# Kernel tuning notes

Measured on AMD Instinct MI355X. Metric: run time of the kernel, lower is better.

## Reference

```python
import jax, jax.numpy as jnp
import numpy as np

NUM_ITERATIONS = 3


def squash(t, axis=-1):
    # scale * t / sqrt(||t||^2 + eps), scale = ||t||^2 / (1 + ||t||^2)
    sq = jnp.sum(t * t, axis=axis, keepdims=True)
    return (sq / (1.0 + sq)) * t / jnp.sqrt(sq + 1e-8)


def setup_inputs() -> dict:
    key = jax.random.key(0)
    k1, k2 = jax.random.split(key)
    B, C, R, I, O = 128, 10, 8192, 8, 16
    x = jax.random.normal(k1, (B, R, I), dtype=jnp.float32)
    route_weights = jax.random.normal(k2, (C, R, I, O), dtype=jnp.float32) * 0.1
    return {"x": x, "route_weights": route_weights}


def reference(x, route_weights):
    # x: [B, R, I]; route_weights: [C, R, I, O]
    u_hat = jnp.einsum('bri,crio->bcro', x, route_weights)  # [B, C, R, O]
    B, C, R, O = u_hat.shape
    b_ij = jnp.zeros((B, C, R), dtype=u_hat.dtype)
    v_j = None
    for it in range(NUM_ITERATIONS):
        c_ij = jax.nn.softmax(b_ij, axis=1)                 # [B, C, R]
        s_j = jnp.einsum('bcr,bcro->bco', c_ij, u_hat)      # [B, C, O]
        v_j = squash(s_j, axis=-1)                          # [B, C, O]
        if it < NUM_ITERATIONS - 1:
            a_ij = jnp.einsum('bcro,bco->bcr', u_hat, v_j)  # [B, C, R]
            b_ij = b_ij + a_ij
    return v_j
```

## Files before the change

kernel.cpp:

```cpp
#include <hip/hip_runtime.h>
#include <hip/hip_fp16.h>
#include <math.h>

#define B_ 128
#define C_ 10
#define R_ 8192
#define I_ 8
#define O_ 16

typedef __attribute__((ext_vector_type(8))) _Float16 half8;
typedef __attribute__((ext_vector_type(16))) float f32x16;

#define XROW 512
#define WROW 64
#define WZERO 80
#define SBO (C_ * B_ * O_)
#define SLOTS 512

__device__ __forceinline__ unsigned pk2(float a, float b) {
    __half2 h = __floats2half2_rn(a, b);
    return *(unsigned*)&h;
}

__global__ __launch_bounds__(512, 4) void fused_iter(const float* __restrict__ x,
                                                     const float* __restrict__ w,
                                                     const float* __restrict__ vsum,
                                                     __half* __restrict__ part,
                                                     int mode) {
    __shared__ unsigned xls[2 * 8 * XROW];
    __shared__ unsigned wls[2 * 81 * WROW];

    const int tid  = threadIdx.x;
    const int wave = tid >> 6;
    const int sg   = wave >> 2;
    const int stid = tid & 255;
    const int lane = tid & 63;
    const int n    = lane & 31;
    const int g    = lane >> 5;
    const int rp_m = (lane & 31) >> 4;
    const int o_m  = lane & 15;
    const int b    = (wave & 3) * 32 + n;
    const int r0   = blockIdx.x * 16 + sg * 8;

    unsigned* const xbase = xls + sg * (8 * XROW);
    unsigned* const wbase = wls + sg * (81 * WROW);
    unsigned* const red_u = xls;

#pragma unroll
    for (int k = 0; k < 8; ++k) {
        const int f = k * 256 + stid;
        const int bb = f >> 4;
        const int rr = (f >> 1) & 7;
        const int q = f & 1;
        const float4 v = *(const float4*)(x + ((size_t)bb * R_ + r0 + rr) * 8 + q * 4);
        *(uint2*)(xbase + rr * XROW + ((bb * 4 + q * 2) ^ (rr << 2))) =
            make_uint2(pk2(v.x, v.y), pk2(v.z, v.w));
    }
#pragma unroll
    for (int k = 0; k < 5; ++k) {
        const int id = k * 256 + stid;
        const int o = id & 15;
        const int r = (id >> 4) & 7;
        const int c = id >> 7;
        const float* wp = w + ((size_t)(c * R_ + r0 + r) * 8) * 16 + o;
        const float f0 = wp[0],  f1 = wp[16],  f2 = wp[32],  f3 = wp[48];
        const float f4 = wp[64], f5 = wp[80],  f6 = wp[96],  f7 = wp[112];
        *(uint4*)(wbase + (c * 8 + r) * WROW + o * 4) =
            make_uint4(pk2(f0, f1), pk2(f2, f3), pk2(f4, f5), pk2(f6, f7));
    }
    if (stid < WROW) wbase[WZERO * WROW + stid] = 0u;
    __syncthreads();

    const int act = (g == rp_m);

    half8 xbr[4];
#pragma unroll
    for (int rp = 0; rp < 4; ++rp) {
        const int row = 2 * rp + g;
        xbr[rp] = *(const half8*)(xbase + row * XROW + ((b * 4) ^ (row << 2)));
    }
    __syncthreads();

    f32x16 zero16;
#pragma unroll
    for (int j = 0; j < 16; ++j) zero16[j] = 0.f;

#define RED_WRITE_AND_FLUSH(A0,A1,A2,A3,A4,A5,A6,A7)                           \
    {                                                                          \
        const int cp = c & 1;                                                  \
        unsigned* rw = red_u + ((cp * 2 + sg) * 128 + b) * 10;                 \
        *(uint2*)(rw + 2 * g)     = make_uint2(pk2(A0, A1), pk2(A2, A3));      \
        *(uint2*)(rw + 4 + 2 * g) = make_uint2(pk2(A4, A5), pk2(A6, A7));      \
        if (cp == 1) {                                                         \
            __syncthreads();                                                   \
            const int cp2 = tid >> 8, t2 = tid & 255;                          \
            const int b2 = t2 >> 1, oh = t2 & 1;                               \
            const int cout = c - 1 + cp2;                                      \
            const unsigned* r0p = red_u + ((cp2 * 2 + 0) * 128 + b2) * 10 + oh * 4; \
            const unsigned* r1p = red_u + ((cp2 * 2 + 1) * 128 + b2) * 10 + oh * 4; \
            const uint2 xa = *(const uint2*)r0p;                               \
            const uint2 xb2 = *(const uint2*)(r0p + 2);                        \
            const uint2 ya = *(const uint2*)r1p;                               \
            const uint2 yb = *(const uint2*)(r1p + 2);                         \
            unsigned ua[4] = {xa.x, xa.y, xb2.x, xb2.y};                       \
            unsigned ub[4] = {ya.x, ya.y, yb.x, yb.y};                         \
            unsigned uo[4];                                                    \
            _Pragma("unroll")                                                  \
            for (int j = 0; j < 4; ++j) {                                      \
                const float2 fa = __half22float2(*(const __half2*)&ua[j]);     \
                const float2 fb = __half22float2(*(const __half2*)&ub[j]);     \
                uo[j] = pk2(fa.x + fb.x, fa.y + fb.y);                         \
            }                                                                  \
            *(uint4*)(part + ((size_t)blockIdx.x * C_ + cout) * (B_ * O_)      \
                      + b2 * O_ + oh * 8) = make_uint4(uo[0], uo[1], uo[2], uo[3]); \
            __syncthreads();                                                   \
        }                                                                      \
    }

    if (mode) {
        float dinv[4];
        {
            float dacc[4] = {0.f, 0.f, 0.f, 0.f};
#pragma unroll 1
            for (int c = 0; c < C_; ++c) {
                const float4* vp = (const float4*)(vsum + ((size_t)c * B_ + b) * O_ + 4 * g);
                const float4 va = vp[0];
                const float4 vb = vp[2];
#pragma unroll
                for (int rp = 0; rp < 4; ++rp) {
                    const int woff = act ? ((c * 8 + 2 * rp + g) * WROW + o_m * 4)
                                         : (WZERO * WROW);
                    const half8 a = *(const half8*)(wbase + woff);
                    const f32x16 u = __builtin_amdgcn_mfma_f32_32x32x16_f16(a, xbr[rp], zero16, 0, 0, 0);
                    const float p0 = u[0] * va.x + u[1] * va.y + u[2] * va.z + u[3] * va.w
                                   + u[4] * vb.x + u[5] * vb.y + u[6] * vb.z + u[7] * vb.w;
                    const float p1 = u[8] * va.x + u[9] * va.y + u[10] * va.z + u[11] * va.w
                                   + u[12] * vb.x + u[13] * vb.y + u[14] * vb.z + u[15] * vb.w;
                    const float send = g ? p0 : p1;
                    const float recv = __shfl_xor(send, 32);
                    const float pg = (g ? p1 : p0) + recv;
                    dacc[rp] += __expf(pg);
                }
            }
#pragma unroll
            for (int rp = 0; rp < 4; ++rp) dinv[rp] = 1.0f / dacc[rp];
        }

#pragma unroll 1
        for (int c = 0; c < C_; ++c) {
            const float4* vp = (const float4*)(vsum + ((size_t)c * B_ + b) * O_ + 4 * g);
            const float4 va = vp[0];
            const float4 vb = vp[2];
            float acc[8];
#pragma unroll
            for (int rp = 0; rp < 4; ++rp) {
                const int woff = act ? ((c * 8 + 2 * rp + g) * WROW + o_m * 4)
                                     : (WZERO * WROW);
                const half8 a = *(const half8*)(wbase + woff);
                const f32x16 u = __builtin_amdgcn_mfma_f32_32x32x16_f16(a, xbr[rp], zero16, 0, 0, 0);
                const float p0 = u[0] * va.x + u[1] * va.y + u[2] * va.z + u[3] * va.w
                               + u[4] * vb.x + u[5] * vb.y + u[6] * vb.z + u[7] * vb.w;
                const float p1 = u[8] * va.x + u[9] * va.y + u[10] * va.z + u[11] * va.w
                               + u[12] * vb.x + u[13] * vb.y + u[14] * vb.z + u[15] * vb.w;
                const float send = g ? p0 : p1;
                const float recv = __shfl_xor(send, 32);
                const float pg = (g ? p1 : p0) + recv;
                const float w_own = __expf(pg) * dinv[rp];
                const float w_oth = __shfl_xor(w_own, 32);
                const float c0 = g ? w_oth : w_own;
                const float c1 = g ? w_own : w_oth;
                if (rp == 0) {
#pragma unroll
                    for (int j = 0; j < 8; ++j) acc[j] = c0 * u[j] + c1 * u[j + 8];
                } else {
#pragma unroll
                    for (int j = 0; j < 8; ++j) acc[j] += c0 * u[j] + c1 * u[j + 8];
                }
            }
            RED_WRITE_AND_FLUSH(acc[0], acc[1], acc[2], acc[3],
                                acc[4], acc[5], acc[6], acc[7]);
        }
    } else {
#pragma unroll 1
        for (int c = 0; c < C_; ++c) {
            f32x16 acc;
#pragma unroll
            for (int rp = 0; rp < 4; ++rp) {
                const int woff = act ? ((c * 8 + 2 * rp + g) * WROW + o_m * 4)
                                     : (WZERO * WROW);
                const half8 a = *(const half8*)(wbase + woff);
                acc = __builtin_amdgcn_mfma_f32_32x32x16_f16(a, xbr[rp],
                                                             rp == 0 ? zero16 : acc, 0, 0, 0);
            }
            const float f0 = (acc[0] + acc[8])  * 0.1f, f1 = (acc[1] + acc[9])  * 0.1f;
            const float f2 = (acc[2] + acc[10]) * 0.1f, f3 = (acc[3] + acc[11]) * 0.1f;
            const float f4 = (acc[4] + acc[12]) * 0.1f, f5 = (acc[5] + acc[13]) * 0.1f;
            const float f6 = (acc[6] + acc[14]) * 0.1f, f7 = (acc[7] + acc[15]) * 0.1f;
            RED_WRITE_AND_FLUSH(f0, f1, f2, f3, f4, f5, f6, f7);
        }
    }
#undef RED_WRITE_AND_FLUSH
}

__global__ __launch_bounds__(512) void finish_fused(const __half* __restrict__ part,
                                                    float* __restrict__ vsum,
                                                    float* __restrict__ out,
                                                    int mode) {
    __shared__ float2 red[16][32];
    const int q  = threadIdx.x >> 5;
    const int pp = threadIdx.x & 31;
    const int pi = blockIdx.x * 32 + pp;

    const unsigned* pu = (const unsigned*)part + (size_t)q * 32 * (SBO / 2) + pi;
    float sx = 0.f, sy = 0.f;
#pragma unroll 8
    for (int s = 0; s < 32; ++s) {
        const unsigned uv = pu[(size_t)s * (SBO / 2)];
        const float2 f = __half22float2(*(const __half2*)&uv);
        sx += f.x; sy += f.y;
    }
    red[q][pp] = make_float2(sx, sy);
    __syncthreads();

    if (threadIdx.x < 32) {
        float2 s2 = red[0][pp];
#pragma unroll
        for (int j = 1; j < 16; ++j) { s2.x += red[j][pp].x; s2.y += red[j][pp].y; }

        float sq = s2.x * s2.x + s2.y * s2.y;
        sq += __shfl_xor(sq, 1);
        sq += __shfl_xor(sq, 2);
        sq += __shfl_xor(sq, 4);
        const float scale = sq / ((1.0f + sq) * sqrtf(sq + 1e-8f));
        const float v0 = scale * s2.x, v1 = scale * s2.y;
        const int t0 = 2 * pi;

        if (mode == 0) {
            *(float2*)(vsum + t0) = make_float2(v0, v1);
        } else if (mode == 1) {
            const float2 old = *(const float2*)(vsum + t0);
            *(float2*)(vsum + t0) = make_float2(old.x + v0, old.y + v1);
        } else {
            const int o = t0 & 15, b = (t0 >> 4) & 127, c = t0 >> 11;
            *(float2*)(out + ((size_t)b * C_ + c) * O_ + o) = make_float2(v0, v1);
        }
    }
}

extern "C" void kernel_launch(void* const* d_in, const int* in_sizes, int n_in,
                              void* d_out, int out_size, void* d_ws, size_t ws_size,
                              hipStream_t stream) {
    const float* x = (const float*)d_in[0];
    const float* w = (const float*)d_in[1];
    float* out = (float*)d_out;

    __half* part = (__half*)d_ws;
    float* vsum  = (float*)(part + (size_t)SLOTS * SBO);

    const dim3 fgrid(R_ / 16);
    const dim3 ggrid(320);

    for (int it = 0; it < 3; ++it) {
        const int mode = (it > 0);
        const int fmode = (it == 2) ? 2 : it;
        fused_iter<<<fgrid, 512, 0, stream>>>(x, w, vsum, part, mode);
        finish_fused<<<ggrid, 512, 0, stream>>>(part, vsum, out, fmode);
    }
}
```

Baseline: 203.7 us.

## Fold routing-weight accumulation into a second MFMA over scaled x inputs

In the routing iterations, the weighted sum over routes is no longer done with per-element FMAs on the u_hat MFMA output. Instead each x fragment is scaled by its fp16 routing coefficient and fed to a second MFMA that accumulates s_j across route pairs. The first iteration switches to a single active MFMA layout so only the first 8 accumulator lanes are summed. This doubles the MFMA count in the routing loop in exchange for removing shuffles and vector FMAs, and it adds fp16 rounding of the coefficient-scaled inputs.

```diff
diff --git a/kernel.cpp b/kernel.cpp
--- a/kernel.cpp
+++ b/kernel.cpp
@@ -72,6 +72,7 @@
     __syncthreads();
 
     const int act = (g == rp_m);
+    const int actf = (rp_m == 0);
 
     half8 xbr[4];
 #pragma unroll
@@ -151,13 +152,13 @@
             const float4* vp = (const float4*)(vsum + ((size_t)c * B_ + b) * O_ + 4 * g);
             const float4 va = vp[0];
             const float4 vb = vp[2];
-            float acc[8];
+            f32x16 sacc;
 #pragma unroll
             for (int rp = 0; rp < 4; ++rp) {
-                const int woff = act ? ((c * 8 + 2 * rp + g) * WROW + o_m * 4)
-                                     : (WZERO * WROW);
-                const half8 a = *(const half8*)(wbase + woff);
-                const f32x16 u = __builtin_amdgcn_mfma_f32_32x32x16_f16(a, xbr[rp], zero16, 0, 0, 0);
+                const int wslot = (c * 8 + 2 * rp + g) * WROW + o_m * 4;
+                const int woff_d = act ? wslot : (WZERO * WROW);
+                const half8 ad = *(const half8*)(wbase + woff_d);
+                const f32x16 u = __builtin_amdgcn_mfma_f32_32x32x16_f16(ad, xbr[rp], zero16, 0, 0, 0);
                 const float p0 = u[0] * va.x + u[1] * va.y + u[2] * va.z + u[3] * va.w
                                + u[4] * vb.x + u[5] * vb.y + u[6] * vb.z + u[7] * vb.w;
                 const float p1 = u[8] * va.x + u[9] * va.y + u[10] * va.z + u[11] * va.w
@@ -166,19 +167,17 @@
                 const float recv = __shfl_xor(send, 32);
                 const float pg = (g ? p1 : p0) + recv;
                 const float w_own = __expf(pg) * dinv[rp];
-                const float w_oth = __shfl_xor(w_own, 32);
-                const float c0 = g ? w_oth : w_own;
-                const float c1 = g ? w_own : w_oth;
-                if (rp == 0) {
-#pragma unroll
-                    for (int j = 0; j < 8; ++j) acc[j] = c0 * u[j] + c1 * u[j + 8];
-                } else {
-#pragma unroll
-                    for (int j = 0; j < 8; ++j) acc[j] += c0 * u[j] + c1 * u[j + 8];
-                }
+                const _Float16 wh = (_Float16)w_own;
+                half8 xc;
+#pragma unroll
+                for (int j = 0; j < 8; ++j) xc[j] = (_Float16)(xbr[rp][j] * wh);
+                const int woff_f = actf ? wslot : (WZERO * WROW);
+                const half8 af = *(const half8*)(wbase + woff_f);
+                sacc = __builtin_amdgcn_mfma_f32_32x32x16_f16(af, xc,
+                                                              rp == 0 ? zero16 : sacc, 0, 0, 0);
             }
-            RED_WRITE_AND_FLUSH(acc[0], acc[1], acc[2], acc[3],
-                                acc[4], acc[5], acc[6], acc[7]);
+            RED_WRITE_AND_FLUSH(sacc[0], sacc[1], sacc[2], sacc[3],
+                                sacc[4], sacc[5], sacc[6], sacc[7]);
         }
     } else {
 #pragma unroll 1
@@ -186,16 +185,16 @@
             f32x16 acc;
 #pragma unroll
             for (int rp = 0; rp < 4; ++rp) {
-                const int woff = act ? ((c * 8 + 2 * rp + g) * WROW + o_m * 4)
-                                     : (WZERO * WROW);
-                const half8 a = *(const half8*)(wbase + woff);
-                acc = __builtin_amdgcn_mfma_f32_32x32x16_f16(a, xbr[rp],
+                const int woff_f = actf ? ((c * 8 + 2 * rp + g) * WROW + o_m * 4)
+                                        : (WZERO * WROW);
+                const half8 af = *(const half8*)(wbase + woff_f);
+                acc = __builtin_amdgcn_mfma_f32_32x32x16_f16(af, xbr[rp],
                                                              rp == 0 ? zero16 : acc, 0, 0, 0);
             }
-            const float f0 = (acc[0] + acc[8])  * 0.1f, f1 = (acc[1] + acc[9])  * 0.1f;
-            const float f2 = (acc[2] + acc[10]) * 0.1f, f3 = (acc[3] + acc[11]) * 0.1f;
-            const float f4 = (acc[4] + acc[12]) * 0.1f, f5 = (acc[5] + acc[13]) * 0.1f;
-            const float f6 = (acc[6] + acc[14]) * 0.1f, f7 = (acc[7] + acc[15]) * 0.1f;
+            const float f0 = acc[0] * 0.1f, f1 = acc[1] * 0.1f;
+            const float f2 = acc[2] * 0.1f, f3 = acc[3] * 0.1f;
+            const float f4 = acc[4] * 0.1f, f5 = acc[5] * 0.1f;
+            const float f6 = acc[6] * 0.1f, f7 = acc[7] * 0.1f;
             RED_WRITE_AND_FLUSH(f0, f1, f2, f3, f4, f5, f6, f7);
         }
     }
```

After: 200.6 us. No clear change (-1.5%).
